# Optimization experiments

Measured on AMD Instinct MI355X. Metric: run time of the kernel, lower is better.

The kernel has to match this reference:

```python
import jax, jax.numpy as jnp
import numpy as np


def _shift(x, k):
    # roll time axis forward by k, zero-filling the first k steps
    if k == 0:
        return x
    return jnp.pad(x, ((0, 0), (k, 0), (0, 0)))[:, : x.shape[1]]


def _stu_conv(u, v, n):
    # u: (B,L,D), v: (L,K) spectral filters; non-tensordot branch of conv()
    B, L, D = u.shape
    K = v.shape[1]
    sgn = jnp.where(jnp.arange(L) % 2 == 1, -1.0, 1.0).astype(jnp.float32)[None, :, None, None]
    ue = jnp.broadcast_to(u[:, :, None, :], (B, L, K, D)).astype(jnp.float32)
    U = jnp.stack([ue, ue * sgn], axis=-1)                     # (B,L,K,D,2)
    Uf = jnp.fft.rfft(U, n=n, axis=1)
    vf = jnp.fft.rfft(v.astype(jnp.float32)[None, :, :, None, None], n=n, axis=1)
    Uc = jnp.fft.irfft(vf * Uf, n=n, axis=1)[:, :L]            # (B,L,K,D,2)
    U_plus = Uc[..., 0]
    U_minus = Uc[..., 1] * sgn
    return U_plus.astype(u.dtype), U_minus.astype(u.dtype)


def setup_inputs() -> dict:
    key = jax.random.key(0)
    ks = jax.random.split(key, 6)
    B, L, D, K, k_u, k_y = 2, 1024, 512, 16, 3, 2
    u = jax.random.normal(ks[0], (B, L, D), jnp.float32)
    filters = jax.random.normal(ks[1], (L, K), jnp.float32) / np.float32(np.sqrt(L))
    M_u = jax.random.normal(ks[2], (D, k_u, D), jnp.float32) * 0.01
    M_y = jax.random.normal(ks[3], (D, k_y, D), jnp.float32) * 0.01
    M_phi_plus = jax.random.normal(ks[4], (K, D, D), jnp.float32) * 0.01
    M_phi_minus = jax.random.normal(ks[5], (K, D, D), jnp.float32) * 0.01
    return {"u": u, "filters": filters, "M_u": M_u, "M_y": M_y,
            "M_phi_plus": M_phi_plus, "M_phi_minus": M_phi_minus}


def reference(u, filters, M_u, M_y, M_phi_plus, M_phi_minus):
    B, L, D = u.shape
    n = 1 << int(np.ceil(np.log2(2 * L - 1)))  # nearest power of two >= 2L-1
    k_u = M_u.shape[1]
    k_y = M_y.shape[1]

    # FFT-based long convolution with the +/- sign trick
    U_plus, U_minus = _stu_conv(u, filters, n)
    spectral = (jnp.einsum('blkd,kdo->blo', U_plus, M_phi_plus)
                + jnp.einsum('blkd,kdo->blo', U_minus, M_phi_minus))

    # input-AR term of compute_ar_strict: sum_j u[t+1-j] @ M_u[:, j-1].T (shifts 0..k_u-1)
    u_sh = jnp.stack([_shift(u, j - 1) for j in range(1, k_u + 1)], axis=1)  # (B,k_u,L,D)
    y_in = jnp.einsum('bjlf,ijf->bli', u_sh, M_u)

    z = spectral + y_in  # (B,L,D)

    # output-AR recurrence of compute_ar_strict as a scan
    def step(y_buf, z_t):
        y_t = z_t + jnp.einsum('bjf,djf->bd', y_buf, M_y)
        y_buf = jnp.concatenate([y_t[:, None], y_buf[:, :-1]], axis=1)
        return y_buf, y_t

    _, ys = jax.lax.scan(step, jnp.zeros((B, k_y, D), z.dtype), jnp.swapaxes(z, 0, 1))
    return jnp.swapaxes(ys, 0, 1)  # (B,L,D)
```

## Files before the change

### kernel.cpp

```cpp
#include <hip/hip_runtime.h>
#include <hip/hip_bf16.h>


using bf16 = __hip_bfloat16;
typedef __attribute__((ext_vector_type(8))) short bf16x8;
typedef __attribute__((ext_vector_type(4))) float f32x4;

#define B_   2
#define L_   1024
#define D_   512
#define K_   16
#define KT   17920
#define ROWS 2048
#define NTAP 6
#define PBLD 3584
#define SPLITD 14
#define SPLITR 6
#define ZBROWS 1032
#define NKS 40
#define NTD 20
#define WZOFF 4194304

#define WAIT_VM6 0x0F76
#define WAIT_VM4 0x0F74
#define WAIT_VM3 0x0F73
#define WAIT_VM0 0x0F70

__device__ __forceinline__ void gll16(const void* g, void* l) {
    __builtin_amdgcn_global_load_lds(
        (const __attribute__((address_space(1))) unsigned int*)g,
        (__attribute__((address_space(3))) unsigned int*)l, 16, 0, 0);
}

__global__ void prep_all(const float* __restrict__ u, const float* __restrict__ fil,
                         const float* __restrict__ Mu, const float* __restrict__ My,
                         const float* __restrict__ Mp, const float* __restrict__ Mm,
                         bf16* __restrict__ U, bf16* __restrict__ BT,
                         bf16* __restrict__ PB, bf16* __restrict__ W,
                         bf16* __restrict__ Myb, bf16* __restrict__ BTT,
                         bf16* __restrict__ uPT) {
    __shared__ bf16 t[64][72];
    int bid = blockIdx.x, tid = threadIdx.x;
    auto pack4 = [](float4 v) {
        ushort4 o; bf16 h;
        h = __float2bfloat16(v.x); o.x = *(unsigned short*)&h;
        h = __float2bfloat16(v.y); o.y = *(unsigned short*)&h;
        h = __float2bfloat16(v.z); o.z = *(unsigned short*)&h;
        h = __float2bfloat16(v.w); o.w = *(unsigned short*)&h;
        return o;
    };
    if (bid < 3072) {
        int e4 = bid * 256 + tid;
        int r = e4 / 384, rem = e4 % 384;
        int tt = rem >> 7, f = (rem & 127) * 4;
        int b = r >> 10, l = r & 1023;
        float4 v = {0.f, 0.f, 0.f, 0.f};
        if (l >= tt) v = *(const float4*)&u[((size_t)b * L_ + l - tt) * D_ + f];
        *(ushort4*)&U[(size_t)r * KT + 16384 + tt * 512 + f] = pack4(v);
    } else if (bid < 3840) {
        int e4 = (bid - 3072) * 256 + tid;
        int o = e4 / 384, tf4 = (e4 % 384) * 4;
        float4 v = *(const float4*)&Mu[(size_t)o * 1536 + tf4];
        *(ushort4*)&BT[(size_t)o * KT + 16384 + tf4] = pack4(v);
    } else if (bid < 4352) {
        int e4 = (bid - 3840) * 256 + tid;
        int n = e4 >> 8, c4 = (e4 & 255) * 4;
        float4 v;
        if (c4 < 512) {
            v.x = (n == c4) ? 1.f : 0.f;     v.y = (n == c4 + 1) ? 1.f : 0.f;
            v.z = (n == c4 + 2) ? 1.f : 0.f; v.w = (n == c4 + 3) ? 1.f : 0.f;
        } else v = *(const float4*)&My[(size_t)n * 1024 + (c4 - 512)];
        *(ushort4*)&PB[(size_t)n * PBLD + c4] = pack4(v);
    } else if (bid < 5120) {
        int tile = bid - 4352;
        int set = tile >> 8, rem = tile & 255;
        int k = rem >> 4, g = (rem >> 2) & 3, kb = rem & 3;
        for (int idx = tid; idx < 4096; idx += 256) {
            int i = idx >> 5, jp = idx & 31;
            int j = ((jp >> 3) ^ ((i >> 1) & 3)) * 8 + (jp & 7);
            int x = g * 128 + i - kb * 32 - j - (set == 2 ? 1 : 0);
            float v = 0.f;
            if (x >= 0) {
                int row = (set == 0) ? 2 * x : 2 * x + 1;
                v = fil[row * K_ + k];
            }
            W[(size_t)tile * 4096 + idx] = __float2bfloat16(v);
        }
    } else if (bid < 5632) {
        int e4 = (bid - 5120) * 256 + tid;
        float4 v = *(const float4*)&My[(size_t)e4 * 4];
        *(ushort4*)&Myb[(size_t)e4 * 4] = pack4(v);
    } else if (bid < 7872) {
        int tt = bid - 5632;
        int zb = tt >> 6, rem = tt & 63;
        int bx = rem & 7, by = rem >> 3;
        int col = tid & 63, r0 = (tid >> 6) * 16;
        if (zb < 32) {
            int dt = bx * 64, ot = by * 64, c = zb;
            int k = c & 15;
            const float* sp = Mp + (size_t)k * D_ * D_;
            const float* sm = Mm + (size_t)k * D_ * D_;
            float sg = (c < 16) ? 1.f : -1.f;
            for (int i = 0; i < 16; ++i) {
                size_t o_ = (size_t)(dt + r0 + i) * D_ + ot + col;
                t[r0 + i][col] = __float2bfloat16(sp[o_] + sg * sm[o_]);
            }
            __syncthreads();
            for (int i = 0; i < 16; ++i)
                BT[(size_t)(ot + r0 + i) * KT + c * D_ + dt + col] = t[col][r0 + i];
        } else if (zb < 34) {
            int h = zb - 32;
            int dt = bx * 64, ft = by * 64;
            for (int i = 0; i < 16; ++i)
                t[r0 + i][col] = __float2bfloat16(My[(size_t)(dt + r0 + i) * 1024 + (1 - h) * 512 + ft + col]);
            __syncthreads();
            for (int i = 0; i < 16; ++i)
                BTT[(size_t)(ft + r0 + i) * 1024 + h * 512 + dt + col] = t[col][r0 + i];
        } else {
            for (int it = 0; it < 4; ++it) {
                int b = it >> 1, p = it & 1;
                int mt = bx * 64, dt = by * 64;
                __syncthreads();
                for (int i = 0; i < 16; ++i)
                    t[r0 + i][col] = __float2bfloat16(u[((size_t)b * L_ + 2 * (mt + r0 + i) + p) * D_ + dt + col]);
                __syncthreads();
                for (int i = 0; i < 16; ++i)
                    uPT[((size_t)it * 512 + dt + r0 + i) * 512 + mt + col] = t[col][r0 + i];
            }
        }
    } else {
        ushort4 z4 = {0, 0, 0, 0};
        for (int i = 0; i < 4; ++i)
            *(ushort4*)&W[(size_t)WZOFF + (size_t)(i * 256 + tid) * 4] = z4;
    }
}

__device__ __forceinline__ void phi_body(
    const bf16* A, int lda, const bf16* BT, int ldb,
    bf16* out, int ldo, int klen, const bf16* add, int lad,
    int row0, int col0, bf16* sA, bf16* sB)
{
    const int tid = threadIdx.x, lane = tid & 63, wave = tid >> 6;
    const int wm = (wave & 1) * 64, wn = (wave >> 1) * 64;
    const int ml = lane & 15, q = lane >> 4;
    const int srow = lane >> 2, scol = (((lane & 3) ^ ((srow >> 1) & 3))) * 8;
    const int swz = ((ml >> 1) & 3);
    f32x4 acc[4][4] = {};

    for (int k = 0; k < klen; k += 32) {
        __syncthreads();
        #pragma unroll
        for (int repi = 0; repi < 2; ++repi) {
            int a = wave + repi * 4;
            gll16(A  + (size_t)(row0 + a * 16 + srow) * lda + k + scol, &sA[a * 512]);
            gll16(BT + (size_t)(col0 + a * 16 + srow) * ldb + k + scol, &sB[a * 512]);
        }
        __syncthreads();
        bf16x8 af[4], bfr[4];
        #pragma unroll
        for (int i = 0; i < 4; ++i)
            af[i] = *(const bf16x8*)&sA[(wm + i * 16 + ml) * 32 + (q ^ swz) * 8];
        #pragma unroll
        for (int j = 0; j < 4; ++j)
            bfr[j] = *(const bf16x8*)&sB[(wn + j * 16 + ml) * 32 + (q ^ swz) * 8];
        #pragma unroll
        for (int i = 0; i < 4; ++i)
            #pragma unroll
            for (int j = 0; j < 4; ++j)
                acc[i][j] = __builtin_amdgcn_mfma_f32_16x16x32_bf16(af[i], bfr[j], acc[i][j], 0, 0, 0);
    }
    #pragma unroll
    for (int i = 0; i < 4; ++i)
        #pragma unroll
        for (int j = 0; j < 4; ++j)
            #pragma unroll
            for (int reg = 0; reg < 4; ++reg) {
                int r = row0 + wm + i * 16 + q * 4 + reg;
                int cc = col0 + wn + j * 16 + ml;
                float v = acc[i][j][reg];
                if (add) v += __bfloat162float(add[(size_t)r * lad + cc]);
                out[(size_t)r * ldo + cc] = __float2bfloat16(v);
            }
}

__device__ __forceinline__ void phi_pipe8(
    const bf16* A, int lda, const bf16* BT, int ldb,
    bf16* out, int ldo, int klen, const bf16* add, int lad,
    int row0, int col0, bf16* sAr, bf16* sBr)
{
    const int tid = threadIdx.x, lane = tid & 63, wave = tid >> 6;
    const int wm = (wave & 1) * 64, wn = (wave >> 1) * 64;
    const int ml = lane & 15, q = lane >> 4;
    const int srow = lane >> 2, scol = (((lane & 3) ^ ((srow >> 1) & 3))) * 8;
    const int swz = ((ml >> 1) & 3);
    f32x4 acc[4][4] = {};

    const bf16* bA  = A  + (size_t)(row0 + wave * 16 + srow) * lda + scol;
    const bf16* bB0 = BT + (size_t)(col0 + (2 * wave) * 16 + srow) * ldb + scol;
    const bf16* bB1 = BT + (size_t)(col0 + (2 * wave + 1) * 16 + srow) * ldb + scol;
    auto stage = [&](int s, int buf) {
        gll16(bA  + s * 32, &sAr[buf * 4096 + wave * 512]);
        gll16(bB0 + s * 32, &sBr[buf * 8192 + (2 * wave) * 512]);
        gll16(bB1 + s * 32, &sBr[buf * 8192 + (2 * wave + 1) * 512]);
    };
    auto compute = [&](int c) {
        bf16x8 af[4], bfr[4];
        #pragma unroll
        for (int i = 0; i < 4; ++i)
            af[i] = *(const bf16x8*)&sAr[c * 4096 + (wm + i * 16 + ml) * 32 + (q ^ swz) * 8];
        #pragma unroll
        for (int j = 0; j < 4; ++j)
            bfr[j] = *(const bf16x8*)&sBr[c * 8192 + (wn + j * 16 + ml) * 32 + (q ^ swz) * 8];
        #pragma unroll
        for (int i = 0; i < 4; ++i)
            #pragma unroll
            for (int j = 0; j < 4; ++j)
                acc[i][j] = __builtin_amdgcn_mfma_f32_16x16x32_bf16(af[i], bfr[j], acc[i][j], 0, 0, 0);
    };
    const int n = klen >> 5;
    stage(0, 0); stage(1, 1);
    int c = 0, nb = 2;
    for (int i = 0; i < n - 1; ++i) {
        __builtin_amdgcn_s_waitcnt(WAIT_VM3);
        __builtin_amdgcn_s_barrier();
        if (i + 2 < n) stage(i + 2, nb);
        compute(c);
        c = (c == 2) ? 0 : c + 1; nb = (nb == 2) ? 0 : nb + 1;
    }
    __builtin_amdgcn_s_waitcnt(WAIT_VM0);
    __builtin_amdgcn_s_barrier();
    compute(c);

    #pragma unroll
    for (int i = 0; i < 4; ++i)
        #pragma unroll
        for (int j = 0; j < 4; ++j)
            #pragma unroll
            for (int reg = 0; reg < 4; ++reg) {
                int r = row0 + wm + i * 16 + q * 4 + reg;
                int cc = col0 + wn + j * 16 + ml;
                float v = acc[i][j][reg];
                if (add) v += __bfloat162float(add[(size_t)r * lad + cc]);
                out[(size_t)r * ldo + cc] = __float2bfloat16(v);
            }
}

__device__ __forceinline__ void mmtile_pipe(
    const bf16* Abase, int lda, const bf16* Bbase, int ldb, int n,
    bf16* o, int ldo, int row0, int col0, bf16 (*sA)[4096], bf16 (*sB)[4096])
{
    const int tid = threadIdx.x, lane = tid & 63, wave = tid >> 6;
    const int wm = (wave & 1) * 64, wn = (wave >> 1) * 64;
    const int ml = lane & 15, q = lane >> 4;
    const int srow = lane >> 2, scol = (((lane & 3) ^ ((srow >> 1) & 3))) * 8;
    const int swz = ((ml >> 1) & 3);
    f32x4 acc[4][4] = {};

    const bf16* bA0 = Abase + (size_t)(wave * 16 + srow) * lda + scol;
    const bf16* bA1 = Abase + (size_t)((wave + 4) * 16 + srow) * lda + scol;
    const bf16* bB0 = Bbase + (size_t)(wave * 16 + srow) * ldb + scol;
    const bf16* bB1 = Bbase + (size_t)((wave + 4) * 16 + srow) * ldb + scol;
    auto stage = [&](int s, int buf) {
        gll16(bA0 + s * 32, &sA[buf][wave * 512]);
        gll16(bA1 + s * 32, &sA[buf][(wave + 4) * 512]);
        gll16(bB0 + s * 32, &sB[buf][wave * 512]);
        gll16(bB1 + s * 32, &sB[buf][(wave + 4) * 512]);
    };
    auto compute = [&](int c) {
        bf16x8 af[4], bfr[4];
        #pragma unroll
        for (int i = 0; i < 4; ++i)
            af[i] = *(const bf16x8*)&sA[c][(wm + i * 16 + ml) * 32 + (q ^ swz) * 8];
        #pragma unroll
        for (int j = 0; j < 4; ++j)
            bfr[j] = *(const bf16x8*)&sB[c][(wn + j * 16 + ml) * 32 + (q ^ swz) * 8];
        #pragma unroll
        for (int i = 0; i < 4; ++i)
            #pragma unroll
            for (int j = 0; j < 4; ++j)
                acc[i][j] = __builtin_amdgcn_mfma_f32_16x16x32_bf16(af[i], bfr[j], acc[i][j], 0, 0, 0);
    };
    stage(0, 0); stage(1, 1);
    int c = 0, nb = 2;
    for (int i = 0; i < n - 1; ++i) {
        __builtin_amdgcn_s_waitcnt(WAIT_VM4);
        __builtin_amdgcn_s_barrier();
        if (i + 2 < n) stage(i + 2, nb);
        compute(c);
        c = (c == 2) ? 0 : c + 1; nb = (nb == 2) ? 0 : nb + 1;
    }
    __builtin_amdgcn_s_waitcnt(WAIT_VM0);
    __builtin_amdgcn_s_barrier();
    compute(c);

    #pragma unroll
    for (int i = 0; i < 4; ++i)
        #pragma unroll
        for (int j = 0; j < 4; ++j)
            #pragma unroll
            for (int reg = 0; reg < 4; ++reg) {
                int r = row0 + wm + i * 16 + q * 4 + reg;
                int cc = col0 + wn + j * 16 + ml;
                o[(size_t)r * ldo + cc] = __float2bfloat16(acc[i][j][reg]);
            }
}

__global__ void k_ztaps(const bf16* __restrict__ partD, float* __restrict__ z,
                        bf16* __restrict__ zbuf, bf16* PB, const bf16* BTT) {
    __shared__ bf16 sA[3][4096];
    __shared__ bf16 sB[3][4096];
    int bid = blockIdx.x;
    if (bid < 32) {
        int row0 = (bid & 3) * 128, col0 = (bid >> 2) * 128;
        mmtile_pipe(PB + 3 * 512 + (size_t)row0 * PBLD, PBLD,
                    BTT + (size_t)col0 * 1024, 1024, 32,
                    PB + 5 * 512, PBLD, row0, col0, sA, sB);
        return;
    }
    if (bid == 32) {
        ushort4 z4 = {0, 0, 0, 0};
        for (int i = 0; i < 8; ++i) {
            int e4 = i * 256 + threadIdx.x;
            int b = e4 >> 10, rem = e4 & 1023;
            int g = rem >> 7, c4 = (rem & 127) * 4;
            *(ushort4*)&zbuf[(size_t)(b * ZBROWS + g) * 512 + c4] = z4;
        }
        return;
    }
    int t = (bid - 33) * 256 + threadIdx.x;
    int r = t >> 7, f4 = (t & 127) * 4;
    const ushort4* p = (const ushort4*)partD;
    float4 s = {0.f, 0.f, 0.f, 0.f};
    #pragma unroll
    for (int c = 0; c < SPLITD; ++c) {
        ushort4 v = p[(size_t)c * (ROWS * D_ / 4) + t];
        s.x += __uint_as_float((unsigned)v.x << 16);
        s.y += __uint_as_float((unsigned)v.y << 16);
        s.z += __uint_as_float((unsigned)v.z << 16);
        s.w += __uint_as_float((unsigned)v.w << 16);
    }
    ((float4*)z)[t] = s;
    ushort4 zb4;
    { bf16 h;
      h = __float2bfloat16(s.x); zb4.x = *(unsigned short*)&h;
      h = __float2bfloat16(s.y); zb4.y = *(unsigned short*)&h;
      h = __float2bfloat16(s.z); zb4.z = *(unsigned short*)&h;
      h = __float2bfloat16(s.w); zb4.w = *(unsigned short*)&h; }
    int b = r >> 10, li = r & 1023;
    *(ushort4*)&zbuf[(size_t)(b * ZBROWS + 8 + li) * 512 + f4] = zb4;
}

__global__ void reduce_out(const float* __restrict__ z, const bf16* __restrict__ partR,
                           float* __restrict__ out) {
    int t = blockIdx.x * 256 + threadIdx.x;
    if (t >= ROWS * D_ / 4) return;
    float4 s = ((const float4*)z)[t];
    const ushort4* p = (const ushort4*)partR;
    #pragma unroll
    for (int c = 0; c < SPLITR; ++c) {
        ushort4 v = p[(size_t)c * (ROWS * D_ / 4) + t];
        s.x += __uint_as_float((unsigned)v.x << 16);
        s.y += __uint_as_float((unsigned)v.y << 16);
        s.z += __uint_as_float((unsigned)v.z << 16);
        s.w += __uint_as_float((unsigned)v.w << 16);
    }
    ((float4*)out)[t] = s;
}

__global__ __launch_bounds__(512, 2) void conv8(
    const bf16* __restrict__ W, const bf16* __restrict__ uPT,
    bf16* __restrict__ U,
    const bf16* PB, const bf16* BTT, const bf16* Myb)
{
    __shared__ bf16 sA[4][8192];
    __shared__ bf16 sB[4][8192];
    int id = blockIdx.x;
    const int tid = threadIdx.x, lane = tid & 63, wave = tid >> 6;
    if (id < 24) {
        int pz = id >> 3, sub = id & 7;
        int row0 = (sub & 3) * 128, col0 = (sub >> 2) * 256;
        bf16* BTTw = (bf16*)BTT; bf16* PBw = (bf16*)PB;
        if (pz == 0)
            phi_pipe8(PB, PBLD, BTT, 1024, PBw + 2 * 512, PBLD, 1024,
                      nullptr, 0, row0, col0, &sA[0][0], &sB[0][0]);
        else if (pz == 1)
            phi_pipe8(BTT + 512, 1024, Myb + 512, 1024,
                      BTTw + (size_t)512 * 1024, 1024, 512,
                      nullptr, 0, row0, col0, &sA[0][0], &sB[0][0]);
        else
            phi_pipe8(BTT + 512, 1024, Myb, 1024,
                      BTTw + (size_t)512 * 1024 + 512, 1024, 512,
                      BTT, 1024, row0, col0, &sA[0][0], &sB[0][0]);
        __syncthreads();
    }
    const int cid = id;
    const int xcd8 = cid & 7, slot = cid >> 3;
    const int plane = xcd8 >> 1, dt2 = xcd8 & 1;
    const int pc = (plane & 1) | ((slot & 1) << 1);
    const int k = slot >> 1;
    const int b = plane >> 1;
    const int p = (pc & 1) ^ (pc >> 1);
    const int set = (pc < 2) ? 0 : (pc == 2 ? 1 : 2);
    const int ch = (pc < 2) ? k : 16 + k;

    const int wm = (wave >> 2) * 128;
    const int wn = (wave & 3) * 64;
    const int ml = lane & 15, q16 = lane >> 4;
    const int srow = lane >> 2, scol = (((lane & 3) ^ ((srow >> 1) & 3))) * 8;
    const int swz = ((ml >> 1) & 3);
    const int koff = (q16 ^ swz) * 8;

    const int a0 = 2 * wave, a1 = a0 + 1;
    const bf16* wbase = W + ((size_t)(set * 16 + k) * 16) * 4096;
    const bf16* wzero = W + (size_t)WZOFF;
    const bf16* bB0 = uPT + ((size_t)plane * 512 + dt2 * 256 + a0 * 16 + srow) * 512 + scol;
    const bf16* bB1 = uPT + ((size_t)plane * 512 + dt2 * 256 + a1 * 16 + srow) * 512 + scol;

    auto do_pass = [&](int mt2p) {
        const int nks = (mt2p + 1) * 8;
        const int NT = nks >> 1;
        const int rb = mt2p * 2 + (a0 >> 3);

        auto stageA = [&](int s) {
            if (s >= nks) return;
            int s4 = s >> 2;
            const bf16* t0 = (rb >= s4)
                ? wbase + (size_t)((rb - s4) * 4 + (s & 3)) * 4096 : wzero;
            gll16(t0 + ((a0 & 7) * 512 + lane * 8), &sA[s & 3][a0 * 512]);
            gll16(t0 + ((a1 & 7) * 512 + lane * 8), &sA[s & 3][a1 * 512]);
        };
        auto stageB = [&](int s) {
            if (s >= nks) return;
            gll16(bB0 + s * 32, &sB[s & 3][a0 * 512]);
            gll16(bB1 + s * 32, &sB[s & 3][a1 * 512]);
        };

        f32x4 acc[8][4] = {};

        stageB(0); stageB(1); stageA(0); stageA(1);
        stageB(2); stageB(3); stageA(2);
        __builtin_amdgcn_s_waitcnt(WAIT_VM6);
        __builtin_amdgcn_s_barrier();

        for (int t = 0; t < NT; ++t) {
            const int u0 = (2 * t) & 3, u1 = u0 + 1;
            bf16x8 bfr[4][2];
            #pragma unroll
            for (int ph = 0; ph < 4; ++ph) {
                bf16x8 af[2][2];
                if (ph == 0) {
                    #pragma unroll
                    for (int fc = 0; fc < 4; ++fc) {
                        bfr[fc][0] = *(const bf16x8*)&sB[u0][(wn + fc * 16 + ml) * 32 + koff];
                        bfr[fc][1] = *(const bf16x8*)&sB[u1][(wn + fc * 16 + ml) * 32 + koff];
                    }
                }
                #pragma unroll
                for (int f2 = 0; f2 < 2; ++f2) {
                    int R = wm + (2 * ph + f2) * 16 + ml;
                    af[f2][0] = *(const bf16x8*)&sA[u0][R * 32 + koff];
                    af[f2][1] = *(const bf16x8*)&sA[u1][R * 32 + koff];
                }
                if (ph == 0)      stageA(2 * t + 3);
                else if (ph == 1) stageB(2 * t + 4);
                else if (ph == 2) stageB(2 * t + 5);
                else              stageA(2 * t + 4);
                __builtin_amdgcn_s_barrier();
                __builtin_amdgcn_s_setprio(1);
                #pragma unroll
                for (int f2 = 0; f2 < 2; ++f2)
                    #pragma unroll
                    for (int fc = 0; fc < 4; ++fc) {
                        acc[2 * ph + f2][fc] = __builtin_amdgcn_mfma_f32_16x16x32_bf16(
                            af[f2][0], bfr[fc][0], acc[2 * ph + f2][fc], 0, 0, 0);
                        acc[2 * ph + f2][fc] = __builtin_amdgcn_mfma_f32_16x16x32_bf16(
                            af[f2][1], bfr[fc][1], acc[2 * ph + f2][fc], 0, 0, 0);
                    }
                __builtin_amdgcn_s_setprio(0);
                if (ph == 3) {
                    if (t < NT - 2)       __builtin_amdgcn_s_waitcnt(WAIT_VM6);
                    else if (t == NT - 2) __builtin_amdgcn_s_waitcnt(WAIT_VM0);
                }
                __builtin_amdgcn_s_barrier();
            }
        }

        #pragma unroll
        for (int i = 0; i < 8; ++i)
            #pragma unroll
            for (int j = 0; j < 4; ++j)
                #pragma unroll
                for (int reg = 0; reg < 4; ++reg) {
                    int mm = mt2p * 256 + wm + i * 16 + q16 * 4 + reg;
                    int l = 2 * mm + p;
                    int d = dt2 * 256 + wn + j * 16 + ml;
                    U[(size_t)(b * L_ + l) * KT + ch * 512 + d] = __float2bfloat16(acc[i][j][reg]);
                }
    };

    do_pass(1);
    do_pass(0);
}

__global__ __launch_bounds__(512, 2) void gemm_d(
    const bf16* __restrict__ U, const bf16* __restrict__ BT,
    bf16* __restrict__ part, const bf16* PB, const bf16* BTT)
{
    __shared__ bf16 sA[4][8192];
    __shared__ bf16 sB[4][8192];
    int id = blockIdx.x;
    const int tid = threadIdx.x, lane = tid & 63, wave = tid >> 6;
    if (id < 32) {
        if (wave >= 4) {
            for (int i = 0; i < 64; ++i) __syncthreads();
            return;
        }
        int r0_ = (id & 3) * 128, c0_ = (id >> 2) * 128;
        phi_body(PB + 512, PBLD, BTT, 1024, (bf16*)PB + 3 * 512, PBLD, 1024,
                 nullptr, 0, r0_, c0_, &sA[0][0], &sB[0][0]);
        return;
    }
    id -= 32;
    const int xsw = id & 7, slot = id >> 3;
    const int w_ = xsw * 28 + slot;
    const int g = w_ >> 3, rtile = w_ & 7;
    const int zz = g >> 1;
    const int row0 = rtile * 256, col0 = (g & 1) * 256;
    const int k0 = zz * (KT / SPLITD);

    const int wm = (wave >> 2) * 128;
    const int wn = (wave & 3) * 64;
    const int ml = lane & 15, q16 = lane >> 4;
    const int srow = lane >> 2, scol = (((lane & 3) ^ ((srow >> 1) & 3))) * 8;
    const int swz = ((ml >> 1) & 3);
    const int koff = (q16 ^ swz) * 8;

    const int a0 = 2 * wave, a1 = 2 * wave + 1;
    const bf16* bA0 = U  + (size_t)(row0 + a0 * 16 + srow) * KT + k0 + scol;
    const bf16* bA1 = U  + (size_t)(row0 + a1 * 16 + srow) * KT + k0 + scol;
    const bf16* bB0 = BT + (size_t)(col0 + a0 * 16 + srow) * KT + k0 + scol;
    const bf16* bB1 = BT + (size_t)(col0 + a1 * 16 + srow) * KT + k0 + scol;
    auto stageA = [&](int s) {
        if (s >= NKS) return;
        gll16(bA0 + s * 32, &sA[s & 3][a0 * 512]);
        gll16(bA1 + s * 32, &sA[s & 3][a1 * 512]);
    };
    auto stageB = [&](int s) {
        if (s >= NKS) return;
        gll16(bB0 + s * 32, &sB[s & 3][a0 * 512]);
        gll16(bB1 + s * 32, &sB[s & 3][a1 * 512]);
    };

    f32x4 acc[8][4] = {};

    stageB(0); stageB(1); stageA(0); stageA(1);
    stageB(2); stageB(3); stageA(2);
    __builtin_amdgcn_s_waitcnt(WAIT_VM6);
    __builtin_amdgcn_s_barrier();

    for (int t = 0; t < NTD; ++t) {
        const int u0 = (2 * t) & 3, u1 = u0 + 1;
        bf16x8 bfr[4][2];
        #pragma unroll
        for (int ph = 0; ph < 4; ++ph) {
            bf16x8 af[2][2];
            if (ph == 0) {
                #pragma unroll
                for (int fc = 0; fc < 4; ++fc) {
                    bfr[fc][0] = *(const bf16x8*)&sB[u0][(wn + fc * 16 + ml) * 32 + koff];
                    bfr[fc][1] = *(const bf16x8*)&sB[u1][(wn + fc * 16 + ml) * 32 + koff];
                }
            }
            #pragma unroll
            for (int f2 = 0; f2 < 2; ++f2) {
                int R = wm + (2 * ph + f2) * 16 + ml;
                af[f2][0] = *(const bf16x8*)&sA[u0][R * 32 + koff];
                af[f2][1] = *(const bf16x8*)&sA[u1][R * 32 + koff];
            }
            if (ph == 0)      stageA(2 * t + 3);
            else if (ph == 1) stageB(2 * t + 4);
            else if (ph == 2) stageB(2 * t + 5);
            else              stageA(2 * t + 4);
            __builtin_amdgcn_s_barrier();
            __builtin_amdgcn_s_setprio(1);
            #pragma unroll
            for (int f2 = 0; f2 < 2; ++f2)
                #pragma unroll
                for (int fc = 0; fc < 4; ++fc) {
                    acc[2 * ph + f2][fc] = __builtin_amdgcn_mfma_f32_16x16x32_bf16(
                        af[f2][0], bfr[fc][0], acc[2 * ph + f2][fc], 0, 0, 0);
                    acc[2 * ph + f2][fc] = __builtin_amdgcn_mfma_f32_16x16x32_bf16(
                        af[f2][1], bfr[fc][1], acc[2 * ph + f2][fc], 0, 0, 0);
                }
            __builtin_amdgcn_s_setprio(0);
            if (ph == 3) {
                if (t < NTD - 2)       __builtin_amdgcn_s_waitcnt(WAIT_VM6);
                else if (t == NTD - 2) __builtin_amdgcn_s_waitcnt(WAIT_VM0);
            }
            __builtin_amdgcn_s_barrier();
        }
    }

    bf16* o = part + (size_t)zz * ROWS * D_;
    #pragma unroll
    for (int i = 0; i < 8; ++i)
        #pragma unroll
        for (int j = 0; j < 4; ++j)
            #pragma unroll
            for (int reg = 0; reg < 4; ++reg) {
                int r = row0 + wm + i * 16 + q16 * 4 + reg;
                int cc = col0 + wn + j * 16 + ml;
                o[(size_t)r * D_ + cc] = __float2bfloat16(acc[i][j][reg]);
            }
}

__global__ __launch_bounds__(256, 3) void gemm_r(
    const bf16* __restrict__ zbuf, const bf16* __restrict__ BT,
    bf16* __restrict__ part)
{
    __shared__ bf16 sA[3][4096];
    __shared__ bf16 sB[3][4096];
    const int row0 = blockIdx.x * 128, col0 = blockIdx.y * 128;
    const int zz = blockIdx.z;
    const int s = 1 + zz;
    const int b = row0 >> 10, li0 = row0 & 1023;
    mmtile_pipe(zbuf + ((size_t)(b * ZBROWS + 8 + li0 - s)) * 512, 512,
                BT + (size_t)col0 * PBLD + (size_t)zz * 512, PBLD,
                16, part + (size_t)zz * ROWS * D_, D_, row0, col0, sA, sB);
}

extern "C" void kernel_launch(void* const* d_in, const int* in_sizes, int n_in,
                              void* d_out, int out_size, void* d_ws, size_t ws_size,
                              hipStream_t stream) {
    const float* u   = (const float*)d_in[0];
    const float* fil = (const float*)d_in[1];
    const float* Mu  = (const float*)d_in[2];
    const float* My  = (const float*)d_in[3];
    const float* Mp  = (const float*)d_in[4];
    const float* Mm  = (const float*)d_in[5];
    float* out = (float*)d_out;

    char* ws = (char*)d_ws;
    size_t off = 0;
    auto alloc = [&](size_t bytes) { void* p = ws + off; off = (off + bytes + 255) & ~(size_t)255; return p; };
    bf16*  U    = (bf16*) alloc((size_t)ROWS * KT * 2);
    bf16*  BT   = (bf16*) alloc((size_t)512 * KT * 2);
    bf16*  PB   = (bf16*) alloc((size_t)512 * PBLD * 2);
    bf16*  BTT  = (bf16*) alloc((size_t)1024 * 1024 * 2);
    bf16*  Myb  = (bf16*) alloc((size_t)512 * 1024 * 2);
    float* z    = (float*)alloc((size_t)ROWS * D_ * 4);
    bf16*  zb   = (bf16*) alloc((size_t)B_ * ZBROWS * 512 * 2);
    char*  region = (char*)alloc((size_t)16 * ROWS * D_ * 2);
    bf16*  W    = (bf16*)region;
    bf16*  uPT  = (bf16*)(region + (size_t)768 * 4096 * 2);
    bf16*  partD = (bf16*)region;
    bf16*  partR = (bf16*)region;

    prep_all<<<7873, 256, 0, stream>>>(u, fil, Mu, My, Mp, Mm,
                                       U, BT, PB, W, Myb, BTT, uPT);

    conv8<<<256, 512, 0, stream>>>(W, uPT, U, PB, BTT, Myb);

    gemm_d<<<256, 512, 0, stream>>>(U, BT, partD, PB, BTT);

    k_ztaps<<<1057, 256, 0, stream>>>(partD, z, zb, PB, BTT);

    gemm_r<<<dim3(16, 4, SPLITR), 256, 0, stream>>>(zb, PB + 512, partR);

    reduce_out<<<(ROWS * D_ / 4 + 255) / 256, 256, 0, stream>>>(z, partR, out);
}
```

Baseline: 250.0 us.

## Split conv8 passes across blocks and fuse two AR taps per gemm_r block

conv8 now launches separate blocks for each of the two M-tile passes, and the phi GEMM blocks return early instead of also running conv work. This spreads the convolution across more blocks so the GPU is better filled. gemm_r accumulates two shifted taps in one tile via a new two-pass mm128_2tap helper, halving SPLITR from 6 to 3. That reduces the partial-sum buffers written and later reduced, at the cost of longer per-block work and fewer gemm_r blocks.

```diff
diff --git a/kernel.cpp b/kernel.cpp
--- a/kernel.cpp
+++ b/kernel.cpp
@@ -15,7 +15,7 @@
 #define NTAP 6
 #define PBLD 3584
 #define SPLITD 14
-#define SPLITR 6
+#define SPLITR 3
 #define ZBROWS 1032
 #define NKS 40
 #define NTD 20
@@ -305,6 +305,74 @@
             }
 }
 
+__device__ __forceinline__ void mm128_2tap(
+    const bf16* A0base, const bf16* A1base, int lda,
+    const bf16* B0base, const bf16* B1base, int ldb, int n,
+    bf16* o, int ldo, int row0, int col0, bf16 (*sA)[4096], bf16 (*sB)[4096])
+{
+    const int tid = threadIdx.x, lane = tid & 63, wave = tid >> 6;
+    const int wm = (wave & 1) * 64, wn = (wave >> 1) * 64;
+    const int ml = lane & 15, q = lane >> 4;
+    const int srow = lane >> 2, scol = (((lane & 3) ^ ((srow >> 1) & 3))) * 8;
+    const int swz = ((ml >> 1) & 3);
+    f32x4 acc[4][4] = {};
+
+    auto compute = [&](int c) {
+        bf16x8 af[4], bfr[4];
+        #pragma unroll
+        for (int i = 0; i < 4; ++i)
+            af[i] = *(const bf16x8*)&sA[c][(wm + i * 16 + ml) * 32 + (q ^ swz) * 8];
+        #pragma unroll
+        for (int j = 0; j < 4; ++j)
+            bfr[j] = *(const bf16x8*)&sB[c][(wn + j * 16 + ml) * 32 + (q ^ swz) * 8];
+        #pragma unroll
+        for (int i = 0; i < 4; ++i)
+            #pragma unroll
+            for (int j = 0; j < 4; ++j)
+                acc[i][j] = __builtin_amdgcn_mfma_f32_16x16x32_bf16(af[i], bfr[j], acc[i][j], 0, 0, 0);
+    };
+
+    #pragma unroll
+    for (int pass = 0; pass < 2; ++pass) {
+        const bf16* Abase = pass ? A1base : A0base;
+        const bf16* Bbase = pass ? B1base : B0base;
+        const bf16* bA0 = Abase + (size_t)(wave * 16 + srow) * lda + scol;
+        const bf16* bA1 = Abase + (size_t)((wave + 4) * 16 + srow) * lda + scol;
+        const bf16* bB0 = Bbase + (size_t)(wave * 16 + srow) * ldb + scol;
+        const bf16* bB1 = Bbase + (size_t)((wave + 4) * 16 + srow) * ldb + scol;
+        auto stage = [&](int s, int buf) {
+            gll16(bA0 + s * 32, &sA[buf][wave * 512]);
+            gll16(bA1 + s * 32, &sA[buf][(wave + 4) * 512]);
+            gll16(bB0 + s * 32, &sB[buf][wave * 512]);
+            gll16(bB1 + s * 32, &sB[buf][(wave + 4) * 512]);
+        };
+        stage(0, 0); stage(1, 1);
+        int c = 0, nb = 2;
+        for (int i = 0; i < n - 1; ++i) {
+            __builtin_amdgcn_s_waitcnt(WAIT_VM4);
+            __builtin_amdgcn_s_barrier();
+            if (i + 2 < n) stage(i + 2, nb);
+            compute(c);
+            c = (c == 2) ? 0 : c + 1; nb = (nb == 2) ? 0 : nb + 1;
+        }
+        __builtin_amdgcn_s_waitcnt(WAIT_VM0);
+        __builtin_amdgcn_s_barrier();
+        compute(c);
+        __syncthreads();
+    }
+
+    #pragma unroll
+    for (int i = 0; i < 4; ++i)
+        #pragma unroll
+        for (int j = 0; j < 4; ++j)
+            #pragma unroll
+            for (int reg = 0; reg < 4; ++reg) {
+                int r = row0 + wm + i * 16 + q * 4 + reg;
+                int cc = col0 + wn + j * 16 + ml;
+                o[(size_t)r * ldo + cc] = __float2bfloat16(acc[i][j][reg]);
+            }
+}
+
 __global__ void k_ztaps(const bf16* __restrict__ partD, float* __restrict__ z,
                         bf16* __restrict__ zbuf, bf16* PB, const bf16* BTT) {
     __shared__ bf16 sA[3][4096];
@@ -391,10 +459,12 @@
             phi_pipe8(BTT + 512, 1024, Myb, 1024,
                       BTTw + (size_t)512 * 1024 + 512, 1024, 512,
                       BTT, 1024, row0, col0, &sA[0][0], &sB[0][0]);
-        __syncthreads();
-    }
-    const int cid = id;
-    const int xcd8 = cid & 7, slot = cid >> 3;
+        return;
+    }
+    const int cid = id - 24;
+    const int mt2 = (cid < 256) ? 1 : 0;
+    const int m = cid & 255;
+    const int xcd8 = m & 7, slot = m >> 3;
     const int plane = xcd8 >> 1, dt2 = xcd8 & 1;
     const int pc = (plane & 1) | ((slot & 1) << 1);
     const int k = slot >> 1;
@@ -402,6 +472,8 @@
     const int p = (pc & 1) ^ (pc >> 1);
     const int set = (pc < 2) ? 0 : (pc == 2 ? 1 : 2);
     const int ch = (pc < 2) ? k : 16 + k;
+    const int nks = (mt2 + 1) * 8;
+    const int NT = nks >> 1;
 
     const int wm = (wave >> 2) * 128;
     const int wn = (wave & 3) * 64;
@@ -411,95 +483,87 @@
     const int koff = (q16 ^ swz) * 8;
 
     const int a0 = 2 * wave, a1 = a0 + 1;
+    const int rb = mt2 * 2 + (a0 >> 3);
     const bf16* wbase = W + ((size_t)(set * 16 + k) * 16) * 4096;
     const bf16* wzero = W + (size_t)WZOFF;
     const bf16* bB0 = uPT + ((size_t)plane * 512 + dt2 * 256 + a0 * 16 + srow) * 512 + scol;
     const bf16* bB1 = uPT + ((size_t)plane * 512 + dt2 * 256 + a1 * 16 + srow) * 512 + scol;
 
-    auto do_pass = [&](int mt2p) {
-        const int nks = (mt2p + 1) * 8;
-        const int NT = nks >> 1;
-        const int rb = mt2p * 2 + (a0 >> 3);
-
-        auto stageA = [&](int s) {
-            if (s >= nks) return;
-            int s4 = s >> 2;
-            const bf16* t0 = (rb >= s4)
-                ? wbase + (size_t)((rb - s4) * 4 + (s & 3)) * 4096 : wzero;
-            gll16(t0 + ((a0 & 7) * 512 + lane * 8), &sA[s & 3][a0 * 512]);
-            gll16(t0 + ((a1 & 7) * 512 + lane * 8), &sA[s & 3][a1 * 512]);
-        };
-        auto stageB = [&](int s) {
-            if (s >= nks) return;
-            gll16(bB0 + s * 32, &sB[s & 3][a0 * 512]);
-            gll16(bB1 + s * 32, &sB[s & 3][a1 * 512]);
-        };
-
-        f32x4 acc[8][4] = {};
-
-        stageB(0); stageB(1); stageA(0); stageA(1);
-        stageB(2); stageB(3); stageA(2);
-        __builtin_amdgcn_s_waitcnt(WAIT_VM6);
-        __builtin_amdgcn_s_barrier();
-
-        for (int t = 0; t < NT; ++t) {
-            const int u0 = (2 * t) & 3, u1 = u0 + 1;
-            bf16x8 bfr[4][2];
-            #pragma unroll
-            for (int ph = 0; ph < 4; ++ph) {
-                bf16x8 af[2][2];
-                if (ph == 0) {
-                    #pragma unroll
-                    for (int fc = 0; fc < 4; ++fc) {
-                        bfr[fc][0] = *(const bf16x8*)&sB[u0][(wn + fc * 16 + ml) * 32 + koff];
-                        bfr[fc][1] = *(const bf16x8*)&sB[u1][(wn + fc * 16 + ml) * 32 + koff];
-                    }
+    auto stageA = [&](int s) {
+        if (s >= nks) return;
+        int s4 = s >> 2;
+        const bf16* t0 = (rb >= s4)
+            ? wbase + (size_t)((rb - s4) * 4 + (s & 3)) * 4096 : wzero;
+        gll16(t0 + ((a0 & 7) * 512 + lane * 8), &sA[s & 3][a0 * 512]);
+        gll16(t0 + ((a1 & 7) * 512 + lane * 8), &sA[s & 3][a1 * 512]);
+    };
+    auto stageB = [&](int s) {
+        if (s >= nks) return;
+        gll16(bB0 + s * 32, &sB[s & 3][a0 * 512]);
+        gll16(bB1 + s * 32, &sB[s & 3][a1 * 512]);
+    };
+
+    f32x4 acc[8][4] = {};
+
+    stageB(0); stageB(1); stageA(0); stageA(1);
+    stageB(2); stageB(3); stageA(2);
+    __builtin_amdgcn_s_waitcnt(WAIT_VM6);
+    __builtin_amdgcn_s_barrier();
+
+    for (int t = 0; t < NT; ++t) {
+        const int u0 = (2 * t) & 3, u1 = u0 + 1;
+        bf16x8 bfr[4][2];
+        #pragma unroll
+        for (int ph = 0; ph < 4; ++ph) {
+            bf16x8 af[2][2];
+            if (ph == 0) {
+                #pragma unroll
+                for (int fc = 0; fc < 4; ++fc) {
+                    bfr[fc][0] = *(const bf16x8*)&sB[u0][(wn + fc * 16 + ml) * 32 + koff];
+                    bfr[fc][1] = *(const bf16x8*)&sB[u1][(wn + fc * 16 + ml) * 32 + koff];
                 }
+            }
+            #pragma unroll
+            for (int f2 = 0; f2 < 2; ++f2) {
+                int R = wm + (2 * ph + f2) * 16 + ml;
+                af[f2][0] = *(const bf16x8*)&sA[u0][R * 32 + koff];
+                af[f2][1] = *(const bf16x8*)&sA[u1][R * 32 + koff];
+            }
+            if (ph == 0)      stageA(2 * t + 3);
+            else if (ph == 1) stageB(2 * t + 4);
+            else if (ph == 2) stageB(2 * t + 5);
+            else              stageA(2 * t + 4);
+            __builtin_amdgcn_s_barrier();
+            __builtin_amdgcn_s_setprio(1);
+            #pragma unroll
+            for (int f2 = 0; f2 < 2; ++f2)
                 #pragma unroll
-                for (int f2 = 0; f2 < 2; ++f2) {
-                    int R = wm + (2 * ph + f2) * 16 + ml;
-                    af[f2][0] = *(const bf16x8*)&sA[u0][R * 32 + koff];
-                    af[f2][1] = *(const bf16x8*)&sA[u1][R * 32 + koff];
+                for (int fc = 0; fc < 4; ++fc) {
+                    acc[2 * ph + f2][fc] = __builtin_amdgcn_mfma_f32_16x16x32_bf16(
+                        af[f2][0], bfr[fc][0], acc[2 * ph + f2][fc], 0, 0, 0);
+                    acc[2 * ph + f2][fc] = __builtin_amdgcn_mfma_f32_16x16x32_bf16(
+                        af[f2][1], bfr[fc][1], acc[2 * ph + f2][fc], 0, 0, 0);
                 }
-                if (ph == 0)      stageA(2 * t + 3);
-                else if (ph == 1) stageB(2 * t + 4);
-                else if (ph == 2) stageB(2 * t + 5);
-                else              stageA(2 * t + 4);
-                __builtin_amdgcn_s_barrier();
-                __builtin_amdgcn_s_setprio(1);
-                #pragma unroll
-                for (int f2 = 0; f2 < 2; ++f2)
-                    #pragma unroll
-                    for (int fc = 0; fc < 4; ++fc) {
-                        acc[2 * ph + f2][fc] = __builtin_amdgcn_mfma_f32_16x16x32_bf16(
-                            af[f2][0], bfr[fc][0], acc[2 * ph + f2][fc], 0, 0, 0);
-                        acc[2 * ph + f2][fc] = __builtin_amdgcn_mfma_f32_16x16x32_bf16(
-                            af[f2][1], bfr[fc][1], acc[2 * ph + f2][fc], 0, 0, 0);
-                    }
-                __builtin_amdgcn_s_setprio(0);
-                if (ph == 3) {
-                    if (t < NT - 2)       __builtin_amdgcn_s_waitcnt(WAIT_VM6);
-                    else if (t == NT - 2) __builtin_amdgcn_s_waitcnt(WAIT_VM0);
-                }
-                __builtin_amdgcn_s_barrier();
-            }
+            __builtin_amdgcn_s_setprio(0);
+            if (ph == 3) {
+                if (t < NT - 2)       __builtin_amdgcn_s_waitcnt(WAIT_VM6);
+                else if (t == NT - 2) __builtin_amdgcn_s_waitcnt(WAIT_VM0);
+            }
+            __builtin_amdgcn_s_barrier();
         }
-
-        #pragma unroll
-        for (int i = 0; i < 8; ++i)
-            #pragma unroll
-            for (int j = 0; j < 4; ++j)
-                #pragma unroll
-                for (int reg = 0; reg < 4; ++reg) {
-                    int mm = mt2p * 256 + wm + i * 16 + q16 * 4 + reg;
-                    int l = 2 * mm + p;
-                    int d = dt2 * 256 + wn + j * 16 + ml;
-                    U[(size_t)(b * L_ + l) * KT + ch * 512 + d] = __float2bfloat16(acc[i][j][reg]);
-                }
-    };
-
-    do_pass(1);
-    do_pass(0);
+    }
+
+    #pragma unroll
+    for (int i = 0; i < 8; ++i)
+        #pragma unroll
+        for (int j = 0; j < 4; ++j)
+            #pragma unroll
+            for (int reg = 0; reg < 4; ++reg) {
+                int mm = mt2 * 256 + wm + i * 16 + q16 * 4 + reg;
+                int l = 2 * mm + p;
+                int d = dt2 * 256 + wn + j * 16 + ml;
+                U[(size_t)(b * L_ + l) * KT + ch * 512 + d] = __float2bfloat16(acc[i][j][reg]);
+            }
 }
 
 __global__ __launch_bounds__(512, 2) void gemm_d(
@@ -622,11 +686,13 @@
     __shared__ bf16 sB[3][4096];
     const int row0 = blockIdx.x * 128, col0 = blockIdx.y * 128;
     const int zz = blockIdx.z;
-    const int s = 1 + zz;
+    const int s0 = 1 + 2 * zz, s1 = 2 + 2 * zz;
     const int b = row0 >> 10, li0 = row0 & 1023;
-    mmtile_pipe(zbuf + ((size_t)(b * ZBROWS + 8 + li0 - s)) * 512, 512,
-                BT + (size_t)col0 * PBLD + (size_t)zz * 512, PBLD,
-                16, part + (size_t)zz * ROWS * D_, D_, row0, col0, sA, sB);
+    mm128_2tap(zbuf + ((size_t)(b * ZBROWS + 8 + li0 - s0)) * 512,
+               zbuf + ((size_t)(b * ZBROWS + 8 + li0 - s1)) * 512, 512,
+               BT + (size_t)col0 * PBLD + (size_t)(2 * zz) * 512,
+               BT + (size_t)col0 * PBLD + (size_t)(2 * zz + 1) * 512, PBLD,
+               16, part + (size_t)zz * ROWS * D_, D_, row0, col0, sA, sB);
 }
 
 extern "C" void kernel_launch(void* const* d_in, const int* in_sizes, int n_in,
@@ -659,7 +725,7 @@
     prep_all<<<7873, 256, 0, stream>>>(u, fil, Mu, My, Mp, Mm,
                                        U, BT, PB, W, Myb, BTT, uPT);
 
-    conv8<<<256, 512, 0, stream>>>(W, uPT, U, PB, BTT, Myb);
+    conv8<<<536, 512, 0, stream>>>(W, uPT, U, PB, BTT, Myb);
 
     gemm_d<<<256, 512, 0, stream>>>(U, BT, partD, PB, BTT);
 
```

Measured after the change: 228.8 us. 1.09x faster.
